# Optimization experiments

Measured on AMD Instinct MI355X. Metric: run time of the kernel, lower is better.

The kernel has to match this reference:

```python
import jax, jax.numpy as jnp
import numpy as np

CLIENT_NUM = 7
NODES_PER_CLIENT = 29
N_NODES = CLIENT_NUM * NODES_PER_CLIENT  # 203


def setup_inputs() -> dict:
    key = jax.random.key(0)
    k1, k2 = jax.random.split(key)
    batch_size = 2048
    output_dim = 256
    globalAdj = jax.random.uniform(k1, (N_NODES, N_NODES), dtype=jnp.float32)
    inputs = jax.random.normal(k2, (NODES_PER_CLIENT, batch_size * output_dim), dtype=jnp.float32)
    return {
        "globalAdj": globalAdj,
        "inputs": inputs,
        "batch_size": batch_size,
        "output_dim": output_dim,
        "id": 3,
    }


def _laplacian_with_self_loop(adj):
    # L = D^{-1/2} (A + I) D^{-1/2}, standard self-loop normalized Laplacian
    a = adj + jnp.eye(adj.shape[0], dtype=adj.dtype)
    d_inv_sqrt = 1.0 / jnp.sqrt(a.sum(axis=1))
    return d_inv_sqrt[:, None] * a * d_inv_sqrt[None, :]


def reference(globalAdj, inputs, batch_size, output_dim, id):
    # Normalized Laplacian recomputed every call (as in the original forward).
    lap = _laplacian_with_self_loop(globalAdj)  # [203, 203]
    # The original Python double-loop over 7x7 blocks followed by per-row list
    # concatenation + stack is exactly the block COLUMN `id` of the Laplacian
    # multiplied by `inputs` -- one fused [203,29] @ [29, B*D] GEMM.
    col = lap[:, id * NODES_PER_CLIENT:(id + 1) * NODES_PER_CLIENT]  # [203, 29]
    out = col @ inputs  # [203, B*D]
    out = out.reshape(N_NODES, batch_size, output_dim)
    return out.transpose(1, 0, 2)  # [B, 203, D]
```

## Files before the change

### kernel.cpp

```cpp
#include <hip/hip_runtime.h>

#define N_NODES 203
#define NPC 29
#define BATCH 2048
#define ODIM 256
#define ROWLEN (BATCH * ODIM)

__global__ __launch_bounds__(256) void lap_col_kernel(
    const float* __restrict__ adj, const int* __restrict__ idp,
    float* __restrict__ col) {
    __shared__ float dinv[N_NODES];
    const int t = threadIdx.x;
    if (t < N_NODES) {
        float s = 1.0f;
        for (int j = 0; j < N_NODES; ++j) s += adj[t * N_NODES + j];
        dinv[t] = 1.0f / sqrtf(s);
    }
    __syncthreads();
    const int base = (*idp) * NPC;
    for (int idx = t; idx < N_NODES * NPC; idx += 256) {
        const int i = idx / NPC;
        const int k = idx - i * NPC;
        const int j = base + k;
        float a = adj[i * N_NODES + j] + (i == j ? 1.0f : 0.0f);
        col[idx] = dinv[i] * a * dinv[j];
    }
}

__global__ __launch_bounds__(256) void gcn_mm_kernel(
    const float* __restrict__ X, const float* __restrict__ col,
    float* __restrict__ out) {
    __shared__ float cl[N_NODES * NPC];
    for (int i = threadIdx.x; i < N_NODES * NPC; i += 256) cl[i] = col[i];
    __syncthreads();

    const int j0 = (blockIdx.x * 256 + threadIdx.x) * 4;
    float4 x[NPC];
#pragma unroll
    for (int k = 0; k < NPC; ++k)
        x[k] = *(const float4*)(X + (size_t)k * ROWLEN + j0);

    const int b = j0 >> 8;
    const int d = j0 & (ODIM - 1);
    float* obase = out + (size_t)b * (N_NODES * ODIM) + d;

    for (int n = 0; n < N_NODES; ++n) {
        float4 acc = {0.f, 0.f, 0.f, 0.f};
        const float* cn = &cl[n * NPC];
#pragma unroll
        for (int k = 0; k < NPC; ++k) {
            const float c = cn[k];
            acc.x += c * x[k].x;
            acc.y += c * x[k].y;
            acc.z += c * x[k].z;
            acc.w += c * x[k].w;
        }
        *(float4*)(obase + n * ODIM) = acc;
    }
}

extern "C" void kernel_launch(void* const* d_in, const int* in_sizes, int n_in,
                              void* d_out, int out_size, void* d_ws, size_t ws_size,
                              hipStream_t stream) {
    const float* adj = (const float*)d_in[0];
    const float* X   = (const float*)d_in[1];
    const int*   idp = (const int*)d_in[4];
    float* out = (float*)d_out;
    float* col = (float*)d_ws;

    lap_col_kernel<<<1, 256, 0, stream>>>(adj, idp, col);

    const int total_j = ROWLEN;
    const int blocks = total_j / (256 * 4);
    gcn_mm_kernel<<<blocks, 256, 0, stream>>>(X, col, out);
}
```

Before: 583.4 us.

## Split node range across grid, narrow per-thread vectors, nontemporal stores, wave-reduced degrees

Each block now handles only half of the output nodes, set by a second grid dimension, and each thread covers two columns instead of four. This gives four times as many blocks and smaller per-thread register and shared-memory footprints, which should raise occupancy. The input X is now read twice, once per node half. Output writes become nontemporal v2f stores, and the degree computation in the Laplacian kernel is parallelised with wave-level shuffle reductions.

```diff
diff --git a/kernel.cpp b/kernel.cpp
--- a/kernel.cpp
+++ b/kernel.cpp
@@ -5,20 +5,26 @@
 #define BATCH 2048
 #define ODIM 256
 #define ROWLEN (BATCH * ODIM)
+#define NSPLIT 2
+#define NCHUNK 102
+
+typedef float v2f __attribute__((ext_vector_type(2)));
 
 __global__ __launch_bounds__(256) void lap_col_kernel(
     const float* __restrict__ adj, const int* __restrict__ idp,
     float* __restrict__ col) {
     __shared__ float dinv[N_NODES];
-    const int t = threadIdx.x;
-    if (t < N_NODES) {
-        float s = 1.0f;
-        for (int j = 0; j < N_NODES; ++j) s += adj[t * N_NODES + j];
-        dinv[t] = 1.0f / sqrtf(s);
+    const int wid = threadIdx.x >> 6, lane = threadIdx.x & 63;
+    for (int r = wid; r < N_NODES; r += 4) {
+        float s = (lane == 0) ? 1.0f : 0.0f;
+        for (int j = lane; j < N_NODES; j += 64) s += adj[r * N_NODES + j];
+#pragma unroll
+        for (int off = 32; off; off >>= 1) s += __shfl_down(s, off);
+        if (lane == 0) dinv[r] = 1.0f / sqrtf(s);
     }
     __syncthreads();
     const int base = (*idp) * NPC;
-    for (int idx = t; idx < N_NODES * NPC; idx += 256) {
+    for (int idx = threadIdx.x; idx < N_NODES * NPC; idx += 256) {
         const int i = idx / NPC;
         const int k = idx - i * NPC;
         const int j = base + k;
@@ -30,32 +36,35 @@
 __global__ __launch_bounds__(256) void gcn_mm_kernel(
     const float* __restrict__ X, const float* __restrict__ col,
     float* __restrict__ out) {
-    __shared__ float cl[N_NODES * NPC];
-    for (int i = threadIdx.x; i < N_NODES * NPC; i += 256) cl[i] = col[i];
+    const int n0 = blockIdx.y * NCHUNK;
+    const int n1 = (n0 + NCHUNK < N_NODES) ? (n0 + NCHUNK) : N_NODES;
+    const int nn = n1 - n0;
+
+    __shared__ float cl[NCHUNK * NPC];
+    for (int i = threadIdx.x; i < nn * NPC; i += 256)
+        cl[i] = col[n0 * NPC + i];
     __syncthreads();
 
-    const int j0 = (blockIdx.x * 256 + threadIdx.x) * 4;
-    float4 x[NPC];
+    const int j0 = (blockIdx.x * 256 + threadIdx.x) * 2;
+    v2f x[NPC];
 #pragma unroll
     for (int k = 0; k < NPC; ++k)
-        x[k] = *(const float4*)(X + (size_t)k * ROWLEN + j0);
+        x[k] = *(const v2f*)(X + (size_t)k * ROWLEN + j0);
 
     const int b = j0 >> 8;
     const int d = j0 & (ODIM - 1);
     float* obase = out + (size_t)b * (N_NODES * ODIM) + d;
 
-    for (int n = 0; n < N_NODES; ++n) {
-        float4 acc = {0.f, 0.f, 0.f, 0.f};
-        const float* cn = &cl[n * NPC];
+    for (int n = n0; n < n1; ++n) {
+        v2f acc = {0.f, 0.f};
+        const float* cn = &cl[(n - n0) * NPC];
 #pragma unroll
         for (int k = 0; k < NPC; ++k) {
             const float c = cn[k];
-            acc.x += c * x[k].x;
-            acc.y += c * x[k].y;
-            acc.z += c * x[k].z;
-            acc.w += c * x[k].w;
+            acc.x = fmaf(c, x[k].x, acc.x);
+            acc.y = fmaf(c, x[k].y, acc.y);
         }
-        *(float4*)(obase + n * ODIM) = acc;
+        __builtin_nontemporal_store(acc, (v2f*)(obase + (size_t)n * ODIM));
     }
 }
 
@@ -70,7 +79,6 @@
 
     lap_col_kernel<<<1, 256, 0, stream>>>(adj, idp, col);
 
-    const int total_j = ROWLEN;
-    const int blocks = total_j / (256 * 4);
-    gcn_mm_kernel<<<blocks, 256, 0, stream>>>(X, col, out);
+    dim3 grid(ROWLEN / (256 * 2), NSPLIT);
+    gcn_mm_kernel<<<grid, 256, 0, stream>>>(X, col, out);
 }
```

After: 576.2 us. No clear change (-1.2%).
